# Performance work log

Measured on AMD Instinct MI355X. Metric: run time of the kernel, lower is better.

The kernel has to match this reference:

```python
import jax, jax.numpy as jnp
import numpy as np

N_NODES = 100000
N_EDGES = 600000
HID = 128
CH_OUT = 3


def setup_inputs() -> dict:
    key = jax.random.key(0)
    ks = jax.random.split(key, 16)
    s = 0.05  # small init to keep tanh in its linear-ish range
    inp = {
        "x": jax.random.normal(ks[0], (N_NODES, HID), dtype=jnp.float32),
        "pos": jax.random.normal(ks[1], (N_NODES, 3), dtype=jnp.float32),
        "edge_index": jax.random.randint(ks[2], (2, N_EDGES), 0, N_NODES, dtype=jnp.int32),
        "fe_w1": jax.random.normal(ks[3], (2 * HID + 1, HID), dtype=jnp.float32) * s,
        "fe_b1": jnp.zeros((HID,), jnp.float32),
        "fe_w2": jax.random.normal(ks[4], (HID, HID), dtype=jnp.float32) * s,
        "fe_b2": jnp.zeros((HID,), jnp.float32),
        "finf_w": jax.random.normal(ks[5], (HID, 1), dtype=jnp.float32) * s,
        "finf_b": jnp.zeros((1,), jnp.float32),
        "fh_w1": jax.random.normal(ks[6], (2 * HID, HID), dtype=jnp.float32) * s,
        "fh_b1": jnp.zeros((HID,), jnp.float32),
        "fh_w2": jax.random.normal(ks[7], (HID, HID), dtype=jnp.float32) * s,
        "fh_b2": jnp.zeros((HID,), jnp.float32),
        "l1_w": jax.random.normal(ks[8], (HID, HID), dtype=jnp.float32) * s,
        "l1_b": jnp.zeros((HID,), jnp.float32),
        "l2_w": jax.random.normal(ks[9], (HID, HID), dtype=jnp.float32) * s,
        "l2_b": jnp.zeros((HID,), jnp.float32),
        "l3_w": jax.random.normal(ks[10], (HID, HID), dtype=jnp.float32) * s,
        "l3_b": jnp.zeros((HID,), jnp.float32),
        "l4_w": jax.random.normal(ks[11], (HID, HID), dtype=jnp.float32) * s,
        "l4_b": jnp.zeros((HID,), jnp.float32),
        "l5_w": jax.random.normal(ks[12], (HID, CH_OUT), dtype=jnp.float32) * s,
        "l5_b": jnp.zeros((CH_OUT,), jnp.float32),
    }
    return inp


def reference(x, pos, edge_index, fe_w1, fe_b1, fe_w2, fe_b2, finf_w, finf_b,
              fh_w1, fh_b1, fh_w2, fh_b2, l1_w, l1_b, l2_w, l2_b, l3_w, l3_b,
              l4_w, l4_b, l5_w, l5_b):
    e_st, e_end = edge_index[0], edge_index[1]
    # dists = ||(pos_i - pos_j)^2||_2  (norm of the squared difference, as in source)
    d = pos[e_st] - pos[e_end]                                  # [E, 3]
    dists = jnp.linalg.norm(jnp.square(d), axis=1, keepdims=True)  # [E, 1]
    # edge MLP f_e
    tmp = jnp.concatenate([x[e_st], x[e_end], dists], axis=1)   # [E, 2H+1]
    m_ij = jnp.tanh(tmp @ fe_w1 + fe_b1)
    m_ij = jnp.tanh(m_ij @ fe_w2 + fe_b2)                        # [E, H]
    # gating f_inf
    e_ij = jnp.tanh(m_ij @ finf_w + finf_b)                      # [E, 1]
    # scatter-sum to source nodes (index_add on edge_index[0])
    m_i = jax.ops.segment_sum(e_ij * m_ij, e_st, num_segments=x.shape[0])  # [N, H]
    # node update f_h with residual
    h = jnp.concatenate([x, m_i], axis=1)                        # [N, 2H]
    x = x + (jnp.tanh(h @ fh_w1 + fh_b1) @ fh_w2 + fh_b2)
    # dense head (dropout p=0.0 is identity)
    lrelu = lambda v: jax.nn.leaky_relu(v, negative_slope=0.01)
    x = lrelu(x @ l1_w + l1_b)
    x = lrelu(x @ l2_w + l2_b)
    x = lrelu(x @ l3_w + l3_b)
    x = lrelu(x @ l4_w + l4_b)
    return x @ l5_w + l5_b
```

## Files before the change

### kernel.cpp

```cpp
#include <hip/hip_runtime.h>
#include <hip/hip_bf16.h>
#include <math.h>

#define HID 128

typedef unsigned short u16;
typedef __attribute__((ext_vector_type(8))) short bfrag;
typedef __attribute__((ext_vector_type(4))) float f32x4;
typedef __attribute__((ext_vector_type(8))) unsigned short u16x8;
typedef __attribute__((ext_vector_type(4))) unsigned short u16x4;

__device__ __forceinline__ float fast_tanh(float v) {
    float e = __expf(2.0f * v);
    float r = __builtin_amdgcn_rcpf(e + 1.0f);
    return 1.0f - 2.0f * r;
}

__device__ __forceinline__ u16 f2b(float f) {
    __hip_bfloat16 h = __float2bfloat16(f);
    return *(u16*)&h;
}
__device__ __forceinline__ float bits2f(unsigned u) {
    union { unsigned u; float f; } v; v.u = u; return v.f;
}

__global__ void __launch_bounds__(256) prep_combo(
    const float* __restrict__ x, u16* __restrict__ xb,
    const float* __restrict__ w1, const float* __restrict__ fh1,
    const float* __restrict__ w2, const float* __restrict__ fh2,
    const float* __restrict__ l1, const float* __restrict__ l2,
    const float* __restrict__ l3, const float* __restrict__ l4,
    u16* __restrict__ w1t, u16* __restrict__ fh1t,
    u16* __restrict__ w2t, u16* __restrict__ fh2t,
    u16* __restrict__ l1t, u16* __restrict__ l2t,
    u16* __restrict__ l3t, u16* __restrict__ l4t,
    const int* __restrict__ est, int* __restrict__ cnt, int E, int nxb)
{
    int b = blockIdx.x, t = threadIdx.x;
    if (b < nxb) {
        int i = b * 256 + t;
        const float4 v0 = *(const float4*)(x + (size_t)i * 8);
        const float4 v1 = *(const float4*)(x + (size_t)i * 8 + 4);
        u16x8 o = { f2b(v0.x), f2b(v0.y), f2b(v0.z), f2b(v0.w),
                    f2b(v1.x), f2b(v1.y), f2b(v1.z), f2b(v1.w) };
        *(u16x8*)(xb + (size_t)i * 8) = o;
        return;
    }
    b -= nxb;
    if (b < 640) {
        const float* src; u16* dst; int K;
        if (b < 256) {
            K = 256;
            if (b < 128) { src = w1;  dst = w1t; }
            else         { src = fh1; dst = fh1t; b -= 128; }
        } else {
            K = 128;
            int s = (b - 256) >> 6; b = (b - 256) & 63;
            switch (s) {
                case 0:  src = w2;  dst = w2t;  break;
                case 1:  src = fh2; dst = fh2t; break;
                case 2:  src = l1;  dst = l1t;  break;
                case 3:  src = l2;  dst = l2t;  break;
                case 4:  src = l3;  dst = l3t;  break;
                default: src = l4;  dst = l4t;  break;
            }
        }
        int idx = b * 256 + t;
        int k = idx >> 7, n = idx & 127;
        dst[(size_t)n * K + k] = f2b(src[(size_t)k * 128 + n]);
        return;
    }
    b -= 640;
    int e = b * 256 + t;
    if (e < E) atomicAdd(&cnt[est[e]], 1);
}

__global__ void __launch_bounds__(256) scan1(const int* __restrict__ cnt,
                                             int* __restrict__ scanout,
                                             int* __restrict__ partial, int N) {
    __shared__ int s[256];
    int t = threadIdx.x, b = blockIdx.x, i = b * 256 + t;
    int v = (i < N) ? cnt[i] : 0;
    s[t] = v; __syncthreads();
#pragma unroll
    for (int d = 1; d < 256; d <<= 1) {
        int add = (t >= d) ? s[t - d] : 0;
        __syncthreads();
        s[t] += add;
        __syncthreads();
    }
    if (i < N) scanout[i] = s[t] - v;
    if (t == 255) partial[b] = s[255];
}

__global__ void __launch_bounds__(512) scan2(int* __restrict__ partial, int NB) {
    __shared__ int s[512];
    int t = threadIdx.x;
    int v = (t < NB) ? partial[t] : 0;
    s[t] = v; __syncthreads();
#pragma unroll
    for (int d = 1; d < 512; d <<= 1) {
        int add = (t >= d) ? s[t - d] : 0;
        __syncthreads();
        s[t] += add;
        __syncthreads();
    }
    if (t < NB) partial[t] = s[t] - v;
}

__global__ void __launch_bounds__(256) scan3(const int* __restrict__ scanout,
                                             const int* __restrict__ partial,
                                             int* __restrict__ offs,
                                             int* __restrict__ cur, int N, int E) {
    int t = threadIdx.x, b = blockIdx.x, i = b * 256 + t;
    if (i < N) { int o = scanout[i] + partial[b]; offs[i] = o; cur[i] = o; }
    if (i == 0) offs[N] = E;
}

__global__ void __launch_bounds__(256) reorder_kernel(const int* __restrict__ est,
                                                      const int* __restrict__ eend,
                                                      int* __restrict__ cur,
                                                      int* __restrict__ est_s,
                                                      int* __restrict__ eend_s, int E) {
    int e = blockIdx.x * 256 + threadIdx.x;
    if (e < E) {
        int s = est[e];
        int p = atomicAdd(&cur[s], 1);
        est_s[p]  = s;
        eend_s[p] = eend[e];
    }
}

template<int KD>
__device__ __forceinline__ void gemm_k(const u16* sbuf, const u16* __restrict__ wt,
                                       int w, int l16, int l4g, f32x4 (&acc)[2][2]) {
    const int RS = KD * 2;
#pragma unroll
    for (int k0 = 0; k0 < KD; k0 += 32) {
        const int kb = k0 * 2 + l4g * 16;
        bfrag a0 = *(const bfrag*)((const char*)sbuf +
                    (unsigned)((l16 * RS + kb) ^ ((l16 & 7) << 4)));
        bfrag a1 = *(const bfrag*)((const char*)sbuf +
                    (unsigned)(((16 + l16) * RS + kb) ^ ((l16 & 7) << 4)));
        bfrag b0 = *(const bfrag*)((const char*)wt + (size_t)(32 * w + l16) * RS + kb);
        bfrag b1 = *(const bfrag*)((const char*)wt + (size_t)(32 * w + 16 + l16) * RS + kb);
        acc[0][0] = __builtin_amdgcn_mfma_f32_16x16x32_bf16(a0, b0, acc[0][0], 0, 0, 0);
        acc[0][1] = __builtin_amdgcn_mfma_f32_16x16x32_bf16(a0, b1, acc[0][1], 0, 0, 0);
        acc[1][0] = __builtin_amdgcn_mfma_f32_16x16x32_bf16(a1, b0, acc[1][0], 0, 0, 0);
        acc[1][1] = __builtin_amdgcn_mfma_f32_16x16x32_bf16(a1, b1, acc[1][1], 0, 0, 0);
    }
}

template<int KD>
__device__ __forceinline__ void gemm_sw(const u16* act, const u16* __restrict__ wt,
                                        int w, int l16, int l4g, f32x4 (&acc)[2][2]) {
    const int RS = KD * 2;
#pragma unroll
    for (int k0 = 0; k0 < KD; k0 += 32) {
        const int kb = k0 * 2 + l4g * 16;
        bfrag wa0 = *(const bfrag*)((const char*)wt + (size_t)(32 * w + l16) * RS + kb);
        bfrag wa1 = *(const bfrag*)((const char*)wt + (size_t)(32 * w + 16 + l16) * RS + kb);
        bfrag be0 = *(const bfrag*)((const char*)act +
                    (unsigned)((l16 * RS + kb) ^ ((l16 & 7) << 4)));
        bfrag be1 = *(const bfrag*)((const char*)act +
                    (unsigned)(((16 + l16) * RS + kb) ^ ((l16 & 7) << 4)));
        acc[0][0] = __builtin_amdgcn_mfma_f32_16x16x32_bf16(wa0, be0, acc[0][0], 0, 0, 0);
        acc[0][1] = __builtin_amdgcn_mfma_f32_16x16x32_bf16(wa0, be1, acc[0][1], 0, 0, 0);
        acc[1][0] = __builtin_amdgcn_mfma_f32_16x16x32_bf16(wa1, be0, acc[1][0], 0, 0, 0);
        acc[1][1] = __builtin_amdgcn_mfma_f32_16x16x32_bf16(wa1, be1, acc[1][1], 0, 0, 0);
    }
}

__global__ void __launch_bounds__(256, 2)
egc_edge_csr(const u16* __restrict__ xb, const float* __restrict__ pos,
             const int* __restrict__ est_s, const int* __restrict__ eend_s,
             const u16* __restrict__ w1t, const float* __restrict__ w1last,
             const float* __restrict__ b1, const u16* __restrict__ w2t,
             const float* __restrict__ b2, const float* __restrict__ fw,
             const float* __restrict__ fb, u16* __restrict__ g,
             float* __restrict__ ev, int n_tiles)
{
    __shared__ __attribute__((aligned(16))) u16 a_sh[2][32 * 256];
    __shared__ __attribute__((aligned(16))) u16 m1_sh[32 * 128];
    __shared__ float red[32][17];
    __shared__ float dist_l[2][32];

    const int t = threadIdx.x, lane = t & 63, w = t >> 6;
    const int l16 = lane & 15, l4g = lane >> 4;
    const unsigned swz = (unsigned)((l16 & 7) << 4);

    bfrag wa10[8], wa11[8], w2f0[4], w2f1[4];
#pragma unroll
    for (int i = 0; i < 8; ++i) {
        int kb = i * 64 + l4g * 16;
        wa10[i] = *(const bfrag*)((const char*)w1t + (size_t)(32 * w + l16) * 512 + kb);
        wa11[i] = *(const bfrag*)((const char*)w1t + (size_t)(32 * w + 16 + l16) * 512 + kb);
    }
#pragma unroll
    for (int i = 0; i < 4; ++i) {
        int kb = i * 64 + l4g * 16;
        w2f0[i] = *(const bfrag*)((const char*)w2t + (size_t)(32 * w + l16) * 256 + kb);
        w2f1[i] = *(const bfrag*)((const char*)w2t + (size_t)(32 * w + 16 + l16) * 256 + kb);
    }
    float w1l_r[2][4], b1_r[2][4], b2_r[2][4], fw_r[2][4];
#pragma unroll
    for (int mi = 0; mi < 2; ++mi)
#pragma unroll
        for (int rg = 0; rg < 4; ++rg) {
            int n = 32 * w + 16 * mi + l4g * 4 + rg;
            w1l_r[mi][rg] = w1last[n];
            b1_r[mi][rg]  = b1[n];
            b2_r[mi][rg]  = b2[n];
            fw_r[mi][rg]  = fw[n];
        }
    const float fbv = fb[0];

    float4 sv0, sv1, sv2, sv3;
    float pax = 0, pay = 0, paz = 0, pbx = 0, pby = 0, pbz = 0;

#define EDGE_ISSUE(TILE) do {                                                  \
        int e0_ = (TILE) * 32;                                                 \
        { int f_ = t;       int e_ = f_ >> 5, q_ = f_ & 31; int ge_ = e0_ + e_;\
          int nd_ = (q_ < 16) ? est_s[ge_] : eend_s[ge_];                      \
          sv0 = *(const float4*)(xb + (size_t)nd_ * 128 + (q_ & 15) * 8); }    \
        { int f_ = t + 256; int e_ = f_ >> 5, q_ = f_ & 31; int ge_ = e0_ + e_;\
          int nd_ = (q_ < 16) ? est_s[ge_] : eend_s[ge_];                      \
          sv1 = *(const float4*)(xb + (size_t)nd_ * 128 + (q_ & 15) * 8); }    \
        { int f_ = t + 512; int e_ = f_ >> 5, q_ = f_ & 31; int ge_ = e0_ + e_;\
          int nd_ = (q_ < 16) ? est_s[ge_] : eend_s[ge_];                      \
          sv2 = *(const float4*)(xb + (size_t)nd_ * 128 + (q_ & 15) * 8); }    \
        { int f_ = t + 768; int e_ = f_ >> 5, q_ = f_ & 31; int ge_ = e0_ + e_;\
          int nd_ = (q_ < 16) ? est_s[ge_] : eend_s[ge_];                      \
          sv3 = *(const float4*)(xb + (size_t)nd_ * 128 + (q_ & 15) * 8); }    \
        if (t < 32) {                                                          \
            int ge_ = e0_ + t;                                                 \
            int a_ = est_s[ge_], b_ = eend_s[ge_];                             \
            pax = pos[a_ * 3]; pay = pos[a_ * 3 + 1]; paz = pos[a_ * 3 + 2];   \
            pbx = pos[b_ * 3]; pby = pos[b_ * 3 + 1]; pbz = pos[b_ * 3 + 2];   \
        }                                                                      \
    } while (0)

#define EDGE_COMMIT(BUF) do {                                                  \
        { int f_ = t;       int e_ = f_ >> 5, q_ = f_ & 31;                    \
          unsigned by_ = (unsigned)(e_ * 512 + q_ * 16) ^ (unsigned)((e_ & 7) << 4); \
          *(float4*)((char*)a_sh[BUF] + by_) = sv0; }                          \
        { int f_ = t + 256; int e_ = f_ >> 5, q_ = f_ & 31;                    \
          unsigned by_ = (unsigned)(e_ * 512 + q_ * 16) ^ (unsigned)((e_ & 7) << 4); \
          *(float4*)((char*)a_sh[BUF] + by_) = sv1; }                          \
        { int f_ = t + 512; int e_ = f_ >> 5, q_ = f_ & 31;                    \
          unsigned by_ = (unsigned)(e_ * 512 + q_ * 16) ^ (unsigned)((e_ & 7) << 4); \
          *(float4*)((char*)a_sh[BUF] + by_) = sv2; }                          \
        { int f_ = t + 768; int e_ = f_ >> 5, q_ = f_ & 31;                    \
          unsigned by_ = (unsigned)(e_ * 512 + q_ * 16) ^ (unsigned)((e_ & 7) << 4); \
          *(float4*)((char*)a_sh[BUF] + by_) = sv3; }                          \
        if (t < 32) {                                                          \
            float dx_ = pax - pbx, dy_ = pay - pby, dz_ = paz - pbz;           \
            dx_ *= dx_; dy_ *= dy_; dz_ *= dz_;                                \
            dist_l[BUF][t] = sqrtf(dx_ * dx_ + dy_ * dy_ + dz_ * dz_);         \
        }                                                                      \
    } while (0)

    int tile = blockIdx.x;
    EDGE_ISSUE(tile);
    int buf = 0;
    int prev_e0 = -1;

    if (tile < n_tiles)
    while (true) {
        EDGE_COMMIT(buf);
        __syncthreads();
        if (prev_e0 >= 0 && t < 32) {
            float s = 0.0f;
#pragma unroll
            for (int j = 0; j < 16; ++j) s += red[t][j];
            ev[prev_e0 + t] = fast_tanh(s + fbv);
        }
        int next = tile + gridDim.x;
        if (next < n_tiles) EDGE_ISSUE(next);
        const int e0 = tile * 32;

        {
            f32x4 acc[2][2] = {};
#pragma unroll
            for (int i = 0; i < 8; ++i) {
                int kb = i * 64 + l4g * 16;
                bfrag be0 = *(const bfrag*)((const char*)a_sh[buf] +
                            ((unsigned)(l16 * 512 + kb) ^ swz));
                bfrag be1 = *(const bfrag*)((const char*)a_sh[buf] +
                            ((unsigned)((16 + l16) * 512 + kb) ^ swz));
                acc[0][0] = __builtin_amdgcn_mfma_f32_16x16x32_bf16(wa10[i], be0, acc[0][0], 0, 0, 0);
                acc[0][1] = __builtin_amdgcn_mfma_f32_16x16x32_bf16(wa10[i], be1, acc[0][1], 0, 0, 0);
                acc[1][0] = __builtin_amdgcn_mfma_f32_16x16x32_bf16(wa11[i], be0, acc[1][0], 0, 0, 0);
                acc[1][1] = __builtin_amdgcn_mfma_f32_16x16x32_bf16(wa11[i], be1, acc[1][1], 0, 0, 0);
            }
            float de0 = dist_l[buf][l16];
            float de1 = dist_l[buf][16 + l16];
#pragma unroll
            for (int mi = 0; mi < 2; ++mi)
#pragma unroll
                for (int ni = 0; ni < 2; ++ni) {
                    float de = ni ? de1 : de0;
                    u16x4 pk;
#pragma unroll
                    for (int rg = 0; rg < 4; ++rg) {
                        float v = fast_tanh(acc[mi][ni][rg] + de * w1l_r[mi][rg] + b1_r[mi][rg]);
                        pk[rg] = f2b(v);
                    }
                    unsigned byte = ((unsigned)((16 * ni + l16) * 256 +
                                     (32 * w + 16 * mi + l4g * 4) * 2)) ^ swz;
                    *(u16x4*)((char*)m1_sh + byte) = pk;
                }
        }
        __syncthreads();

        {
            f32x4 acc[2][2] = {};
#pragma unroll
            for (int i = 0; i < 4; ++i) {
                int kb = i * 64 + l4g * 16;
                bfrag me0 = *(const bfrag*)((const char*)m1_sh +
                            ((unsigned)(l16 * 256 + kb) ^ swz));
                bfrag me1 = *(const bfrag*)((const char*)m1_sh +
                            ((unsigned)((16 + l16) * 256 + kb) ^ swz));
                acc[0][0] = __builtin_amdgcn_mfma_f32_16x16x32_bf16(w2f0[i], me0, acc[0][0], 0, 0, 0);
                acc[0][1] = __builtin_amdgcn_mfma_f32_16x16x32_bf16(w2f0[i], me1, acc[0][1], 0, 0, 0);
                acc[1][0] = __builtin_amdgcn_mfma_f32_16x16x32_bf16(w2f1[i], me0, acc[1][0], 0, 0, 0);
                acc[1][1] = __builtin_amdgcn_mfma_f32_16x16x32_bf16(w2f1[i], me1, acc[1][1], 0, 0, 0);
            }
            float part0 = 0.0f, part1 = 0.0f;
#pragma unroll
            for (int mi = 0; mi < 2; ++mi)
#pragma unroll
                for (int ni = 0; ni < 2; ++ni) {
                    u16x4 pk;
                    float ps = 0.0f;
#pragma unroll
                    for (int rg = 0; rg < 4; ++rg) {
                        float v = fast_tanh(acc[mi][ni][rg] + b2_r[mi][rg]);
                        ps += v * fw_r[mi][rg];
                        pk[rg] = f2b(v);
                    }
                    if (ni) part1 += ps; else part0 += ps;
                    int dstrow = e0 + 16 * ni + l16;
                    *(u16x4*)(g + (size_t)dstrow * 128 + (32 * w + 16 * mi + l4g * 4)) = pk;
                }
            red[l16][w * 4 + l4g]      = part0;
            red[16 + l16][w * 4 + l4g] = part1;
        }

        prev_e0 = e0;
        tile = next; buf ^= 1;
        if (tile >= n_tiles) break;
    }
    __syncthreads();
    if (prev_e0 >= 0 && t < 32) {
        float s = 0.0f;
#pragma unroll
        for (int j = 0; j < 16; ++j) s += red[t][j];
        ev[prev_e0 + t] = fast_tanh(s + fbv);
    }
#undef EDGE_ISSUE
#undef EDGE_COMMIT
}

__global__ void __launch_bounds__(256, 8)
gather_seq(const u16* __restrict__ g, const float* __restrict__ ev,
           const int* __restrict__ offs, u16* __restrict__ m_i)
{
    const int lane = threadIdx.x & 63;
    const int half = lane >> 5;
    const int l32  = lane & 31;
    const int n = blockIdx.x * 4 + (threadIdx.x >> 6);
    const int beg = offs[n], end = offs[n + 1];
    float a0 = 0.0f, a1 = 0.0f, a2 = 0.0f, a3 = 0.0f;
    float b0 = 0.0f, b1 = 0.0f, b2 = 0.0f, b3 = 0.0f;
    int e = beg + half;
    for (; e + 3 < end; e += 4) {
        uint2 v0 = *(const uint2*)(g + (size_t)e * 128 + l32 * 4);
        uint2 v1 = *(const uint2*)(g + (size_t)(e + 2) * 128 + l32 * 4);
        float e0 = ev[e], e1 = ev[e + 2];
        a0 += e0 * bits2f(v0.x << 16);
        a1 += e0 * bits2f(v0.x & 0xFFFF0000u);
        a2 += e0 * bits2f(v0.y << 16);
        a3 += e0 * bits2f(v0.y & 0xFFFF0000u);
        b0 += e1 * bits2f(v1.x << 16);
        b1 += e1 * bits2f(v1.x & 0xFFFF0000u);
        b2 += e1 * bits2f(v1.y << 16);
        b3 += e1 * bits2f(v1.y & 0xFFFF0000u);
    }
    for (; e < end; e += 2) {
        uint2 v0 = *(const uint2*)(g + (size_t)e * 128 + l32 * 4);
        float e0 = ev[e];
        a0 += e0 * bits2f(v0.x << 16);
        a1 += e0 * bits2f(v0.x & 0xFFFF0000u);
        a2 += e0 * bits2f(v0.y << 16);
        a3 += e0 * bits2f(v0.y & 0xFFFF0000u);
    }
    a0 += b0; a1 += b1; a2 += b2; a3 += b3;
    a0 += __shfl_xor(a0, 32);
    a1 += __shfl_xor(a1, 32);
    a2 += __shfl_xor(a2, 32);
    a3 += __shfl_xor(a3, 32);
    if (half == 0) {
        uint2 o;
        o.x = (unsigned)f2b(a0) | ((unsigned)f2b(a1) << 16);
        o.y = (unsigned)f2b(a2) | ((unsigned)f2b(a3) << 16);
        *(uint2*)(m_i + (size_t)n * 128 + l32 * 4) = o;
    }
}

__global__ void __launch_bounds__(256, 3)
egc_edge_mfma(const u16* __restrict__ xb, const float* __restrict__ pos,
              const int* __restrict__ est, const int* __restrict__ eend,
              const u16* __restrict__ w1t, const float* __restrict__ w1last,
              const float* __restrict__ b1, const u16* __restrict__ w2t,
              const float* __restrict__ b2, const float* __restrict__ fw,
              const float* __restrict__ fb, float* __restrict__ m_i)
{
    __shared__ __attribute__((aligned(16))) u16 a_sh[32 * 256];
    __shared__ __attribute__((aligned(16))) u16 m1_sh[32 * 128];
    __shared__ float m2_sh[32][132];
    __shared__ float dist_l[32];
    __shared__ float ev_l[32];
    __shared__ int   st_l[32];

    const int t = threadIdx.x;
    const int e0 = blockIdx.x * 32;
    const int lane = t & 63;
    const int w = t >> 6;
    const int l16 = lane & 15, l4g = lane >> 4;

#pragma unroll
    for (int i = 0; i < 4; ++i) {
        int f = t + 256 * i;
        int e = f >> 5, q = f & 31;
        int ge = e0 + e;
        int node = (q < 16) ? est[ge] : eend[ge];
        float4 v = *(const float4*)(xb + (size_t)node * 128 + (q & 15) * 8);
        unsigned byte = (unsigned)(e * 512 + q * 16) ^ (unsigned)((e & 7) << 4);
        *(float4*)((char*)a_sh + byte) = v;
    }
    if (t < 32) {
        int ge = e0 + t;
        int a = est[ge], b = eend[ge];
        st_l[t] = a;
        float dx = pos[a * 3 + 0] - pos[b * 3 + 0];
        float dy = pos[a * 3 + 1] - pos[b * 3 + 1];
        float dz = pos[a * 3 + 2] - pos[b * 3 + 2];
        dx *= dx; dy *= dy; dz *= dz;
        dist_l[t] = sqrtf(dx * dx + dy * dy + dz * dz);
    }
    __syncthreads();

    {
        f32x4 acc[2][2] = {};
        gemm_k<256>(a_sh, w1t, w, l16, l4g, acc);
#pragma unroll
        for (int mi = 0; mi < 2; ++mi)
#pragma unroll
            for (int ni = 0; ni < 2; ++ni) {
                const int col = 32 * w + 16 * ni + l16;
                const float wl = w1last[col], bb = b1[col];
#pragma unroll
                for (int rg = 0; rg < 4; ++rg) {
                    const int row = 16 * mi + l4g * 4 + rg;
                    float v = fast_tanh(acc[mi][ni][rg] + dist_l[row] * wl + bb);
                    unsigned byte = (unsigned)((row * 256 + col * 2) ^ ((row & 7) << 4));
                    *(u16*)((char*)m1_sh + byte) = f2b(v);
                }
            }
    }
    __syncthreads();

    {
        f32x4 acc[2][2] = {};
        gemm_k<128>(m1_sh, w2t, w, l16, l4g, acc);
#pragma unroll
        for (int mi = 0; mi < 2; ++mi)
#pragma unroll
            for (int ni = 0; ni < 2; ++ni) {
                const int col = 32 * w + 16 * ni + l16;
                const float bb = b2[col];
#pragma unroll
                for (int rg = 0; rg < 4; ++rg) {
                    const int row = 16 * mi + l4g * 4 + rg;
                    m2_sh[row][col] = fast_tanh(acc[mi][ni][rg] + bb);
                }
            }
    }
    __syncthreads();

    if (t < 128) {
        int e = t >> 2, p = t & 3;
        float s = 0.0f;
#pragma unroll
        for (int k = 0; k < 32; ++k) s += m2_sh[e][p * 32 + k] * fw[p * 32 + k];
        s += __shfl_xor(s, 1);
        s += __shfl_xor(s, 2);
        if (p == 0) ev_l[e] = fast_tanh(s + fb[0]);
    }
    __syncthreads();

    {
        int e = t >> 3, l8 = t & 7;
        float ev = ev_l[e];
        size_t base = (size_t)st_l[e] * HID + l8;
#pragma unroll
        for (int i = 0; i < 16; ++i)
            unsafeAtomicAdd(m_i + base + 8 * i, ev * m2_sh[e][l8 + 8 * i]);
    }
}

#define NODE_LAYER_SW(SRC, KD, WT, BIAS, DST, ACT)                             \
    {                                                                          \
        f32x4 acc[2][2] = {};                                                  \
        gemm_sw<KD>(SRC, WT, w, l16, l4g, acc);                                \
        float bbr[2][4];                                                       \
        _Pragma("unroll")                                                      \
        for (int mi = 0; mi < 2; ++mi)                                         \
            _Pragma("unroll")                                                  \
            for (int rg = 0; rg < 4; ++rg)                                     \
                bbr[mi][rg] = (BIAS)[32 * w + 16 * mi + l4g * 4 + rg];         \
        _Pragma("unroll")                                                      \
        for (int mi = 0; mi < 2; ++mi)                                         \
            _Pragma("unroll")                                                  \
            for (int ni = 0; ni < 2; ++ni) {                                   \
                const int node = 16 * ni + l16;                                \
                const int ch = 32 * w + 16 * mi + l4g * 4;                     \
                u16x4 pk;                                                      \
                _Pragma("unroll")                                              \
                for (int rg = 0; rg < 4; ++rg) {                               \
                    float v = acc[mi][ni][rg] + bbr[mi][rg];                   \
                    ACT;                                                       \
                    pk[rg] = f2b(v);                                           \
                }                                                              \
                unsigned byte = ((unsigned)(node * 256 + ch * 2)) ^ swz;       \
                *(u16x4*)((char*)(DST) + byte) = pk;                           \
            }                                                                  \
    }

template<int MODE>
__global__ void __launch_bounds__(256, 4)
egc_node_mfma(const u16* __restrict__ xb, const float* __restrict__ xf,
              const void* __restrict__ m_i,
              const u16* __restrict__ fh1t, const float* __restrict__ hb1,
              const u16* __restrict__ fh2t, const float* __restrict__ hb2,
              const u16* __restrict__ l1t, const float* __restrict__ l1b,
              const u16* __restrict__ l2t, const float* __restrict__ l2b,
              const u16* __restrict__ l3t, const float* __restrict__ l3b,
              const u16* __restrict__ l4t, const float* __restrict__ l4b,
              const float* __restrict__ l5w, const float* __restrict__ l5b,
              float* __restrict__ out)
{
    __shared__ __attribute__((aligned(16))) u16 a_sh[32 * 256];
    __shared__ __attribute__((aligned(16))) u16 bA[32 * 128];
    __shared__ __attribute__((aligned(16))) u16 bB[32 * 128];
    __shared__ float red[32][3][17];

    const int t = threadIdx.x;
    const int n0 = blockIdx.x * 32;
    const int lane = t & 63;
    const int w = t >> 6;
    const int l16 = lane & 15, l4g = lane >> 4;
    const unsigned swz = (unsigned)((l16 & 7) << 4);

#pragma unroll
    for (int i = 0; i < 2; ++i) {
        int f = t + 256 * i;
        int n = f >> 4, q = f & 15;
        float4 v = *(const float4*)(xb + (size_t)(n0 + n) * 128 + q * 8);
        unsigned byte = (unsigned)((n * 512 + q * 16) ^ ((n & 7) << 4));
        *(float4*)((char*)a_sh + byte) = v;
    }
    if (MODE == 0) {
#pragma unroll
        for (int i = 0; i < 2; ++i) {
            int f = t + 256 * i;
            int n = f >> 4, q = f & 15;
            float4 v = *(const float4*)((const u16*)m_i + (size_t)(n0 + n) * 128 + q * 8);
            unsigned byte = (unsigned)((n * 512 + 256 + q * 16) ^ ((n & 7) << 4));
            *(float4*)((char*)a_sh + byte) = v;
        }
    } else {
#pragma unroll
        for (int i = 0; i < 2; ++i) {
            int f = t + 256 * i;
            int n = f >> 4, q = f & 15;
            const float* src = (const float*)m_i + (size_t)(n0 + n) * 128 + q * 8;
            float4 v0 = *(const float4*)(src);
            float4 v1 = *(const float4*)(src + 4);
            u16x8 o = { f2b(v0.x), f2b(v0.y), f2b(v0.z), f2b(v0.w),
                        f2b(v1.x), f2b(v1.y), f2b(v1.z), f2b(v1.w) };
            unsigned byte = (unsigned)((n * 512 + 256 + q * 16) ^ ((n & 7) << 4));
            *(u16x8*)((char*)a_sh + byte) = o;
        }
    }
    __syncthreads();

    NODE_LAYER_SW(a_sh, 256, fh1t, hb1, bA, { v = fast_tanh(v); })
    __syncthreads();

    {
        f32x4 acc[2][2] = {};
        gemm_sw<128>(bA, fh2t, w, l16, l4g, acc);
        float bbr[2][4];
#pragma unroll
        for (int mi = 0; mi < 2; ++mi)
#pragma unroll
            for (int rg = 0; rg < 4; ++rg)
                bbr[mi][rg] = hb2[32 * w + 16 * mi + l4g * 4 + rg];
#pragma unroll
        for (int mi = 0; mi < 2; ++mi)
#pragma unroll
            for (int ni = 0; ni < 2; ++ni) {
                const int node = 16 * ni + l16;
                const int ch = 32 * w + 16 * mi + l4g * 4;
                float4 xr = *(const float4*)(xf + (size_t)(n0 + node) * 128 + ch);
                u16x4 pk;
                pk[0] = f2b(acc[mi][ni][0] + bbr[mi][0] + xr.x);
                pk[1] = f2b(acc[mi][ni][1] + bbr[mi][1] + xr.y);
                pk[2] = f2b(acc[mi][ni][2] + bbr[mi][2] + xr.z);
                pk[3] = f2b(acc[mi][ni][3] + bbr[mi][3] + xr.w);
                unsigned byte = ((unsigned)(node * 256 + ch * 2)) ^ swz;
                *(u16x4*)((char*)bB + byte) = pk;
            }
    }
    __syncthreads();

    NODE_LAYER_SW(bB, 128, l1t, l1b, bA, { v = v > 0.0f ? v : 0.01f * v; })
    __syncthreads();
    NODE_LAYER_SW(bA, 128, l2t, l2b, bB, { v = v > 0.0f ? v : 0.01f * v; })
    __syncthreads();
    NODE_LAYER_SW(bB, 128, l3t, l3b, bA, { v = v > 0.0f ? v : 0.01f * v; })
    __syncthreads();

    {
        f32x4 acc[2][2] = {};
        gemm_sw<128>(bA, l4t, w, l16, l4g, acc);
        float bbr[2][4], w5[2][4][3];
#pragma unroll
        for (int mi = 0; mi < 2; ++mi)
#pragma unroll
            for (int rg = 0; rg < 4; ++rg) {
                int ch = 32 * w + 16 * mi + l4g * 4 + rg;
                bbr[mi][rg] = l4b[ch];
#pragma unroll
                for (int cc = 0; cc < 3; ++cc) w5[mi][rg][cc] = l5w[ch * 3 + cc];
            }
#pragma unroll
        for (int ni = 0; ni < 2; ++ni) {
            float p0 = 0.0f, p1 = 0.0f, p2 = 0.0f;
#pragma unroll
            for (int mi = 0; mi < 2; ++mi)
#pragma unroll
                for (int rg = 0; rg < 4; ++rg) {
                    float v = acc[mi][ni][rg] + bbr[mi][rg];
                    v = v > 0.0f ? v : 0.01f * v;
                    p0 += v * w5[mi][rg][0];
                    p1 += v * w5[mi][rg][1];
                    p2 += v * w5[mi][rg][2];
                }
            const int n = 16 * ni + l16, j = w * 4 + l4g;
            red[n][0][j] = p0;
            red[n][1][j] = p1;
            red[n][2][j] = p2;
        }
    }
    __syncthreads();

    if (t < 96) {
        int n = t / 3, cc = t % 3;
        float s = l5b[cc];
#pragma unroll
        for (int j = 0; j < 16; ++j) s += red[n][cc][j];
        out[(size_t)(n0 + n) * 3 + cc] = s;
    }
}

extern "C" void kernel_launch(void* const* d_in, const int* in_sizes, int n_in,
                              void* d_out, int out_size, void* d_ws, size_t ws_size,
                              hipStream_t stream)
{
    const float* x      = (const float*)d_in[0];
    const float* pos    = (const float*)d_in[1];
    const int*   eidx   = (const int*)d_in[2];
    const float* fe_w1  = (const float*)d_in[3];
    const float* fe_b1  = (const float*)d_in[4];
    const float* fe_w2  = (const float*)d_in[5];
    const float* fe_b2  = (const float*)d_in[6];
    const float* finf_w = (const float*)d_in[7];
    const float* finf_b = (const float*)d_in[8];
    const float* fh_w1  = (const float*)d_in[9];
    const float* fh_b1  = (const float*)d_in[10];
    const float* fh_w2  = (const float*)d_in[11];
    const float* fh_b2  = (const float*)d_in[12];
    const float* l1w    = (const float*)d_in[13];
    const float* l1b    = (const float*)d_in[14];
    const float* l2w    = (const float*)d_in[15];
    const float* l2b    = (const float*)d_in[16];
    const float* l3w    = (const float*)d_in[17];
    const float* l3b    = (const float*)d_in[18];
    const float* l4w    = (const float*)d_in[19];
    const float* l4b    = (const float*)d_in[20];
    const float* l5w    = (const float*)d_in[21];
    const float* l5b    = (const float*)d_in[22];
    float* out = (float*)d_out;

    const int n_edges = in_sizes[2] / 2;
    const int n_nodes = in_sizes[0] / HID;
    const int nsb     = (n_nodes + 255) / 256;
    const int n_tiles = n_edges / 32;
    const int nxb     = (n_nodes * HID) / (256 * 8);
    const int nhb     = (n_edges + 255) / 256;

    char* ws = (char*)d_ws;
    const bool use_csr = (ws_size >= 208800000ULL);

    if (use_csr) {
        u16* g     = (u16*)(ws + 0);
        u16* xb    = (u16*)(ws + 153600000);
        u16* m_i   = (u16*)(ws + 179200000);
        int* est_s  = (int*)(ws + 179200000);
        int* eend_s = (int*)(ws + 181600000);
        u16* w1t  = (u16*)(ws + 204800000);
        u16* w2t  = (u16*)(ws + 204865536);
        u16* fh1t = (u16*)(ws + 204898304);
        u16* fh2t = (u16*)(ws + 204963840);
        u16* l1t  = (u16*)(ws + 204996608);
        u16* l2t  = (u16*)(ws + 205029376);
        u16* l3t  = (u16*)(ws + 205062144);
        u16* l4t  = (u16*)(ws + 205094912);
        int* cnt  = (int*)(ws + 205127680);
        int* offs = (int*)(ws + 205527680);
        int* cur  = (int*)(ws + 205927696);
        float* ev = (float*)(ws + 206327696);
        int* part = (int*)(ws + 208727696);

        (void)hipMemsetAsync(cnt, 0, (size_t)n_nodes * sizeof(int), stream);
        prep_combo<<<dim3(nxb + 640 + nhb), dim3(256), 0, stream>>>(
            x, xb, fe_w1, fh_w1, fe_w2, fh_w2, l1w, l2w, l3w, l4w,
            w1t, fh1t, w2t, fh2t, l1t, l2t, l3t, l4t, eidx, cnt, n_edges, nxb);

        scan1<<<dim3(nsb), dim3(256), 0, stream>>>(cnt, cnt, part, n_nodes);
        scan2<<<dim3(1), dim3(512), 0, stream>>>(part, nsb);
        scan3<<<dim3(nsb), dim3(256), 0, stream>>>(cnt, part, offs, cur, n_nodes, n_edges);
        reorder_kernel<<<dim3(nhb), dim3(256), 0, stream>>>(
            eidx, eidx + n_edges, cur, est_s, eend_s, n_edges);

        egc_edge_csr<<<dim3(512), dim3(256), 0, stream>>>(
            xb, pos, est_s, eend_s, w1t, fe_w1 + (size_t)256 * HID, fe_b1,
            w2t, fe_b2, finf_w, finf_b, g, ev, n_tiles);

        gather_seq<<<dim3(n_nodes / 4), dim3(256), 0, stream>>>(g, ev, offs, m_i);

        egc_node_mfma<0><<<dim3(n_nodes / 32), dim3(256), 0, stream>>>(
            xb, x, m_i, fh1t, fh_b1, fh2t, fh_b2, l1t, l1b, l2t, l2b,
            l3t, l3b, l4t, l4b, l5w, l5b, out);
    } else {
        float* m_i = (float*)(ws + 0);
        u16* xb    = (u16*)(ws + 51200000);
        u16* w1t   = (u16*)(ws + 76800000);
        u16* w2t   = (u16*)(ws + 76865536);
        u16* fh1t  = (u16*)(ws + 76898304);
        u16* fh2t  = (u16*)(ws + 76963840);
        u16* l1t   = (u16*)(ws + 76996608);
        u16* l2t   = (u16*)(ws + 77029376);
        u16* l3t   = (u16*)(ws + 77062144);
        u16* l4t   = (u16*)(ws + 77094912);

        (void)hipMemsetAsync(m_i, 0, (size_t)n_nodes * HID * sizeof(float), stream);
        prep_combo<<<dim3(nxb + 640), dim3(256), 0, stream>>>(
            x, xb, fe_w1, fh_w1, fe_w2, fh_w2, l1w, l2w, l3w, l4w,
            w1t, fh1t, w2t, fh2t, l1t, l2t, l3t, l4t, eidx, (int*)d_ws, 0, nxb);

        egc_edge_mfma<<<dim3(n_edges / 32), dim3(256), 0, stream>>>(
            xb, pos, eidx, eidx + n_edges, w1t, fe_w1 + (size_t)256 * HID, fe_b1,
            w2t, fe_b2, finf_w, finf_b, m_i);

        egc_node_mfma<1><<<dim3(n_nodes / 32), dim3(256), 0, stream>>>(
            xb, x, m_i, fh1t, fh_b1, fh2t, fh_b2, l1t, l1b, l2t, l2b,
            l3t, l3b, l4t, l4b, l5w, l5b, out);
    }
}
```

Before: 344.2 us.

## Software-pipeline edge MLP so GEMM2 of previous tile overlaps GEMM1 of current

Restructures the persistent edge loop into a three-stage software pipeline: each iteration runs GEMM1 for the current tile and GEMM2 for the previous tile, then reduces the gate for the tile before that. m1_sh and the reduction buffer are double-buffered, which removes one __syncthreads per tile and gives the scheduler independent MFMA work to interleave. It costs more shared memory, which may affect the 2-blocks-per-CU occupancy, and adds prologue and epilogue logic. The initial guard for blocks with no tiles (tile >= n_tiles) is gone.

```diff
diff --git a/kernel.cpp b/kernel.cpp
--- a/kernel.cpp
+++ b/kernel.cpp
@@ -181,8 +181,8 @@
              float* __restrict__ ev, int n_tiles)
 {
     __shared__ __attribute__((aligned(16))) u16 a_sh[2][32 * 256];
-    __shared__ __attribute__((aligned(16))) u16 m1_sh[32 * 128];
-    __shared__ float red[32][17];
+    __shared__ __attribute__((aligned(16))) u16 m1_sh[2][32 * 128];
+    __shared__ float red[2][32][17];
     __shared__ float dist_l[2][32];
 
     const int t = threadIdx.x, lane = t & 63, w = t >> 6;
@@ -260,105 +260,107 @@
         }                                                                      \
     } while (0)
 
-    int tile = blockIdx.x;
-    EDGE_ISSUE(tile);
-    int buf = 0;
-    int prev_e0 = -1;
-
-    if (tile < n_tiles)
+    auto do_gemm1 = [&](int p) {
+        f32x4 acc[2][2] = {};
+#pragma unroll
+        for (int i = 0; i < 8; ++i) {
+            int kb = i * 64 + l4g * 16;
+            bfrag be0 = *(const bfrag*)((const char*)a_sh[p] +
+                        ((unsigned)(l16 * 512 + kb) ^ swz));
+            bfrag be1 = *(const bfrag*)((const char*)a_sh[p] +
+                        ((unsigned)((16 + l16) * 512 + kb) ^ swz));
+            acc[0][0] = __builtin_amdgcn_mfma_f32_16x16x32_bf16(wa10[i], be0, acc[0][0], 0, 0, 0);
+            acc[0][1] = __builtin_amdgcn_mfma_f32_16x16x32_bf16(wa10[i], be1, acc[0][1], 0, 0, 0);
+            acc[1][0] = __builtin_amdgcn_mfma_f32_16x16x32_bf16(wa11[i], be0, acc[1][0], 0, 0, 0);
+            acc[1][1] = __builtin_amdgcn_mfma_f32_16x16x32_bf16(wa11[i], be1, acc[1][1], 0, 0, 0);
+        }
+        float de0 = dist_l[p][l16];
+        float de1 = dist_l[p][16 + l16];
+#pragma unroll
+        for (int mi = 0; mi < 2; ++mi)
+#pragma unroll
+            for (int ni = 0; ni < 2; ++ni) {
+                float de = ni ? de1 : de0;
+                u16x4 pk;
+#pragma unroll
+                for (int rg = 0; rg < 4; ++rg) {
+                    float v = fast_tanh(acc[mi][ni][rg] + de * w1l_r[mi][rg] + b1_r[mi][rg]);
+                    pk[rg] = f2b(v);
+                }
+                unsigned byte = ((unsigned)((16 * ni + l16) * 256 +
+                                 (32 * w + 16 * mi + l4g * 4) * 2)) ^ swz;
+                *(u16x4*)((char*)m1_sh[p] + byte) = pk;
+            }
+    };
+
+    auto do_gemm2 = [&](int e0, int rp, int mp) {
+        f32x4 acc[2][2] = {};
+#pragma unroll
+        for (int i = 0; i < 4; ++i) {
+            int kb = i * 64 + l4g * 16;
+            bfrag me0 = *(const bfrag*)((const char*)m1_sh[mp] +
+                        ((unsigned)(l16 * 256 + kb) ^ swz));
+            bfrag me1 = *(const bfrag*)((const char*)m1_sh[mp] +
+                        ((unsigned)((16 + l16) * 256 + kb) ^ swz));
+            acc[0][0] = __builtin_amdgcn_mfma_f32_16x16x32_bf16(w2f0[i], me0, acc[0][0], 0, 0, 0);
+            acc[0][1] = __builtin_amdgcn_mfma_f32_16x16x32_bf16(w2f0[i], me1, acc[0][1], 0, 0, 0);
+            acc[1][0] = __builtin_amdgcn_mfma_f32_16x16x32_bf16(w2f1[i], me0, acc[1][0], 0, 0, 0);
+            acc[1][1] = __builtin_amdgcn_mfma_f32_16x16x32_bf16(w2f1[i], me1, acc[1][1], 0, 0, 0);
+        }
+        float part0 = 0.0f, part1 = 0.0f;
+#pragma unroll
+        for (int mi = 0; mi < 2; ++mi)
+#pragma unroll
+            for (int ni = 0; ni < 2; ++ni) {
+                u16x4 pk;
+                float ps = 0.0f;
+#pragma unroll
+                for (int rg = 0; rg < 4; ++rg) {
+                    float v = fast_tanh(acc[mi][ni][rg] + b2_r[mi][rg]);
+                    ps += v * fw_r[mi][rg];
+                    pk[rg] = f2b(v);
+                }
+                if (ni) part1 += ps; else part0 += ps;
+                int dstrow = e0 + 16 * ni + l16;
+                *(u16x4*)(g + (size_t)dstrow * 128 + (32 * w + 16 * mi + l4g * 4)) = pk;
+            }
+        red[rp][l16][w * 4 + l4g]      = part0;
+        red[rp][16 + l16][w * 4 + l4g] = part1;
+    };
+
+    auto do_reduce = [&](int e0, int rp) {
+        if (t < 32) {
+            float s = 0.0f;
+#pragma unroll
+            for (int j = 0; j < 16; ++j) s += red[rp][t][j];
+            ev[e0 + t] = fast_tanh(s + fbv);
+        }
+    };
+
+    int t1 = blockIdx.x;
+    int t2 = -1, tr = -1;
+    int pk = 0;
+    EDGE_ISSUE(t1);
+    EDGE_COMMIT(0);
+    int tnext = t1 + gridDim.x;
+
     while (true) {
-        EDGE_COMMIT(buf);
         __syncthreads();
-        if (prev_e0 >= 0 && t < 32) {
-            float s = 0.0f;
-#pragma unroll
-            for (int j = 0; j < 16; ++j) s += red[t][j];
-            ev[prev_e0 + t] = fast_tanh(s + fbv);
-        }
-        int next = tile + gridDim.x;
-        if (next < n_tiles) EDGE_ISSUE(next);
-        const int e0 = tile * 32;
-
-        {
-            f32x4 acc[2][2] = {};
-#pragma unroll
-            for (int i = 0; i < 8; ++i) {
-                int kb = i * 64 + l4g * 16;
-                bfrag be0 = *(const bfrag*)((const char*)a_sh[buf] +
-                            ((unsigned)(l16 * 512 + kb) ^ swz));
-                bfrag be1 = *(const bfrag*)((const char*)a_sh[buf] +
-                            ((unsigned)((16 + l16) * 512 + kb) ^ swz));
-                acc[0][0] = __builtin_amdgcn_mfma_f32_16x16x32_bf16(wa10[i], be0, acc[0][0], 0, 0, 0);
-                acc[0][1] = __builtin_amdgcn_mfma_f32_16x16x32_bf16(wa10[i], be1, acc[0][1], 0, 0, 0);
-                acc[1][0] = __builtin_amdgcn_mfma_f32_16x16x32_bf16(wa11[i], be0, acc[1][0], 0, 0, 0);
-                acc[1][1] = __builtin_amdgcn_mfma_f32_16x16x32_bf16(wa11[i], be1, acc[1][1], 0, 0, 0);
-            }
-            float de0 = dist_l[buf][l16];
-            float de1 = dist_l[buf][16 + l16];
-#pragma unroll
-            for (int mi = 0; mi < 2; ++mi)
-#pragma unroll
-                for (int ni = 0; ni < 2; ++ni) {
-                    float de = ni ? de1 : de0;
-                    u16x4 pk;
-#pragma unroll
-                    for (int rg = 0; rg < 4; ++rg) {
-                        float v = fast_tanh(acc[mi][ni][rg] + de * w1l_r[mi][rg] + b1_r[mi][rg]);
-                        pk[rg] = f2b(v);
-                    }
-                    unsigned byte = ((unsigned)((16 * ni + l16) * 256 +
-                                     (32 * w + 16 * mi + l4g * 4) * 2)) ^ swz;
-                    *(u16x4*)((char*)m1_sh + byte) = pk;
-                }
-        }
-        __syncthreads();
-
-        {
-            f32x4 acc[2][2] = {};
-#pragma unroll
-            for (int i = 0; i < 4; ++i) {
-                int kb = i * 64 + l4g * 16;
-                bfrag me0 = *(const bfrag*)((const char*)m1_sh +
-                            ((unsigned)(l16 * 256 + kb) ^ swz));
-                bfrag me1 = *(const bfrag*)((const char*)m1_sh +
-                            ((unsigned)((16 + l16) * 256 + kb) ^ swz));
-                acc[0][0] = __builtin_amdgcn_mfma_f32_16x16x32_bf16(w2f0[i], me0, acc[0][0], 0, 0, 0);
-                acc[0][1] = __builtin_amdgcn_mfma_f32_16x16x32_bf16(w2f0[i], me1, acc[0][1], 0, 0, 0);
-                acc[1][0] = __builtin_amdgcn_mfma_f32_16x16x32_bf16(w2f1[i], me0, acc[1][0], 0, 0, 0);
-                acc[1][1] = __builtin_amdgcn_mfma_f32_16x16x32_bf16(w2f1[i], me1, acc[1][1], 0, 0, 0);
-            }
-            float part0 = 0.0f, part1 = 0.0f;
-#pragma unroll
-            for (int mi = 0; mi < 2; ++mi)
-#pragma unroll
-                for (int ni = 0; ni < 2; ++ni) {
-                    u16x4 pk;
-                    float ps = 0.0f;
-#pragma unroll
-                    for (int rg = 0; rg < 4; ++rg) {
-                        float v = fast_tanh(acc[mi][ni][rg] + b2_r[mi][rg]);
-                        ps += v * fw_r[mi][rg];
-                        pk[rg] = f2b(v);
-                    }
-                    if (ni) part1 += ps; else part0 += ps;
-                    int dstrow = e0 + 16 * ni + l16;
-                    *(u16x4*)(g + (size_t)dstrow * 128 + (32 * w + 16 * mi + l4g * 4)) = pk;
-                }
-            red[l16][w * 4 + l4g]      = part0;
-            red[16 + l16][w * 4 + l4g] = part1;
-        }
-
-        prev_e0 = e0;
-        tile = next; buf ^= 1;
-        if (tile >= n_tiles) break;
-    }
-    __syncthreads();
-    if (prev_e0 >= 0 && t < 32) {
-        float s = 0.0f;
-#pragma unroll
-        for (int j = 0; j < 16; ++j) s += red[t][j];
-        ev[prev_e0 + t] = fast_tanh(s + fbv);
-    }
+        if (tr >= 0) do_reduce(tr * 32, pk ^ 1);
+        bool have_next = (tnext < n_tiles);
+        if (have_next) EDGE_ISSUE(tnext);
+        do_gemm1(pk);
+        if (t2 >= 0) do_gemm2(t2 * 32, pk, pk ^ 1);
+        if (have_next) EDGE_COMMIT(pk ^ 1);
+        tr = t2; t2 = t1;
+        if (!have_next) break;
+        t1 = tnext; tnext += gridDim.x; pk ^= 1;
+    }
+    __syncthreads();
+    if (tr >= 0) do_reduce(tr * 32, pk);
+    do_gemm2(t2 * 32, pk ^ 1, pk);
+    __syncthreads();
+    do_reduce(t2 * 32, pk ^ 1);
 #undef EDGE_ISSUE
 #undef EDGE_COMMIT
 }
```

Result: no change. 341.5 us (-0.8%).
